# Kernel optimization log

Measured on AMD Instinct MI355X. Metric: run time of the kernel, lower is better.

## Reference

```python
import jax, jax.numpy as jnp
import numpy as np

MIN_, MAX_, KSZ, IGNORE_IDX = 10, 10, 3, -255
B, H, W = 256, 256, 256
LI_MAX_ITERS = 64


def setup_inputs() -> dict:
    key = jax.random.key(0)
    x = jax.random.uniform(key, (B, 1, H, W), dtype=jnp.float32)
    return {"x": x}


def _otsu(hist):
    # hist: [256] counts. Returns Otsu threshold (bin value); fg = img > t.
    bins = jnp.arange(256, dtype=jnp.float32)
    w0 = jnp.cumsum(hist)[:-1]
    w1 = hist.sum() - w0
    s0 = jnp.cumsum(hist * bins)[:-1]
    s_tot = (hist * bins).sum()
    m0 = s0 / jnp.maximum(w0, 1e-12)
    m1 = (s_tot - s0) / jnp.maximum(w1, 1e-12)
    var_b = w0 * w1 * (m0 - m1) ** 2
    return jnp.argmax(var_b).astype(jnp.float32)


def _li(hist, init_t):
    # Histogram-based Li iterative minimum cross-entropy threshold
    # (skimage.filters.threshold_li with initial_guess=init_t).
    bins = jnp.arange(256, dtype=jnp.float32)
    img_min = jnp.min(jnp.where(hist > 0, bins, 255.0))
    vals = bins - img_min  # shift so values >= 0 (as skimage does)
    csum = jnp.cumsum(hist)
    cvsum = jnp.cumsum(hist * vals)
    n_tot, s_tot = csum[-1], cvsum[-1]
    tol = 0.5  # integer image -> half the minimal value spacing

    def body(state):
        t_curr, _, i = state
        # background: img <= t_curr + img_min
        idx = jnp.clip(jnp.floor(t_curr + img_min).astype(jnp.int32), 0, 255)
        n_back, s_back = csum[idx], cvsum[idx]
        n_fore, s_fore = n_tot - n_back, s_tot - s_back
        mean_back = jnp.where(n_back > 0, s_back / jnp.maximum(n_back, 1.0), 0.0)
        mean_fore = s_fore / jnp.maximum(n_fore, 1.0)
        eps = 1e-12
        t_next = (mean_back - mean_fore) / (
            jnp.log(jnp.maximum(mean_back, eps)) - jnp.log(jnp.maximum(mean_fore, eps)))
        t_next = jnp.where(mean_back < eps, mean_fore / 2.0, t_next)
        return (t_next, t_curr, i + 1)

    def cond(state):
        t_curr, t_prev, i = state
        return (jnp.abs(t_curr - t_prev) > tol) & (i < LI_MAX_ITERS)

    t0 = init_t - img_min
    t_fin, _, _ = jax.lax.while_loop(cond, body, (t0, t0 + 10.0, 0))
    return t_fin + img_min


def _sample_mask(key, region, k):
    # Uniform sampling without replacement of up to k pixels from region
    # (bool [H,W]) via random-score top-k (equiv. to torch.multinomial
    # with uniform probs, w/o replacement).
    flat = region.reshape(-1)
    scores = jnp.where(flat, jax.random.uniform(key, (flat.shape[0],)), -1.0)
    top, idx = jax.lax.top_k(scores, k)
    valid = (top >= 0.0).astype(jnp.int32)
    mask = jnp.zeros(flat.shape[0], jnp.int32).at[idx].max(valid)
    return mask.reshape(region.shape)


def _dilate(m):
    # kornia dilation with ones (KSZ,KSZ) kernel on a 0/1 mask == max filter.
    return jax.lax.reduce_window(m, 0, jax.lax.max, (KSZ, KSZ), (1, 1), "SAME")


def _per_image(img_u8, key_fg, key_bg):
    # img_u8: [H,W] int32 in [0,255]
    hist = jnp.zeros(256, jnp.float32).at[img_u8.ravel()].add(1.0)
    otsu = jnp.clip(_otsu(hist), 1.0, 254.0)  # clamp 0->1, 255->254
    li_t = _li(hist, otsu)
    roi = img_u8.astype(jnp.float32) > li_t

    fg = _sample_mask(key_fg, roi, MAX_)
    bg = _sample_mask(key_bg, jnp.logical_not(roi), MIN_)
    if KSZ > 1:
        fg = _dilate(fg)
        bg = _dilate(bg)

    overlap = (fg + bg) == 2
    fg = jnp.where(overlap, 0, fg)
    bg = jnp.where(overlap, 0, bg)

    seeds = jnp.full((H, W), IGNORE_IDX, jnp.int32)
    seeds = jnp.where(bg == 1, 0, seeds)
    seeds = jnp.where(fg == 1, 1, seeds)
    return seeds


def reference(x):
    b = x.shape[0]
    # (cam*255).astype(uint8): truncation, cam in [0,1]
    img = jnp.clip(jnp.floor(x[:, 0] * 255.0), 0, 255).astype(jnp.int32)
    keys = jax.random.split(jax.random.key(1), (b, 2))
    return jax.vmap(_per_image)(img, keys[:, 0], keys[:, 1])
```

## Files before the change

kernel.cpp:

```cpp
#include <hip/hip_runtime.h>
#include <stdint.h>

#define NPIX 65536
#define IGN (-255)
#define CAP 768
#define HPART 16384
#define SCRI4 4608

__device__ __forceinline__ uint32_t rotl32(uint32_t v, uint32_t r){ return (v<<r)|(v>>(32u-r)); }

__device__ __forceinline__ void tf2x32(uint32_t k0, uint32_t k1, uint32_t x0, uint32_t x1,
                                       uint32_t &o0, uint32_t &o1){
  uint32_t k2 = k0 ^ k1 ^ 0x1BD11BDAu;
  x0 += k0; x1 += k1;
#define TFR(r) { x0 += x1; x1 = rotl32(x1,(r)); x1 ^= x0; }
  TFR(13u) TFR(15u) TFR(26u) TFR(6u)   x0 += k1; x1 += k2 + 1u;
  TFR(17u) TFR(29u) TFR(16u) TFR(24u)  x0 += k2; x1 += k0 + 2u;
  TFR(13u) TFR(15u) TFR(26u) TFR(6u)   x0 += k0; x1 += k1 + 3u;
  TFR(17u) TFR(29u) TFR(16u) TFR(24u)  x0 += k1; x1 += k2 + 4u;
  TFR(13u) TFR(15u) TFR(26u) TFR(6u)   x0 += k2; x1 += k0 + 5u;
#undef TFR
  o0 = x0; o1 = x1;
}

__device__ __forceinline__ unsigned long long packCand(uint32_t bits, uint32_t pix){
  float f = __uint_as_float((bits >> 9) | 0x3f800000u) - 1.0f;
  uint32_t u = __float_as_uint(f) ^ 0x80000000u;
  return ((unsigned long long)u << 32) | (unsigned long long)(0xFFFFFFFFu - pix);
}

__device__ __forceinline__ void t10_insert(unsigned long long* l, unsigned long long c){
  if (c > l[9]) {
    l[9] = c;
#pragma unroll
    for (int i = 9; i > 0; --i){
      unsigned long long a = l[i-1], b2 = l[i];
      if (b2 > a){ l[i-1] = b2; l[i] = a; }
    }
  }
}

__global__ __launch_bounds__(256, 8)
void k1_stream(const float* __restrict__ x, int* __restrict__ out){
  const int blk = blockIdx.x;
  const int b = blk >> 3, j8 = blk & 7;
  const int tid = threadIdx.x;
  const float4* x4 = (const float4*)(x + (size_t)b * NPIX);
  int* base = out + (size_t)b * NPIX;
  int4* o4 = (int4*)base;

  __shared__ uint32_t histR[1024];
#pragma unroll
  for (int k = 0; k < 4; ++k) histR[tid + 256*k] = 0u;
  __syncthreads();

  const int4 f4 = make_int4(IGN, IGN, IGN, IGN);
  const uint32_t c4 = (uint32_t)(tid & 3);
#pragma unroll
  for (int jj = 0; jj < 8; ++jj){
    int i4 = j8*2048 + jj*256 + tid;
    float4 v = x4[i4];
    uint32_t u0 = (uint32_t)min(max((int)floorf(v.x*255.0f),0),255);
    uint32_t u1 = (uint32_t)min(max((int)floorf(v.y*255.0f),0),255);
    uint32_t u2 = (uint32_t)min(max((int)floorf(v.z*255.0f),0),255);
    uint32_t u3 = (uint32_t)min(max((int)floorf(v.w*255.0f),0),255);
    base[i4] = (int)(u0 | (u1<<8) | (u2<<16) | (u3<<24));
    if (i4 >= SCRI4) o4[i4] = f4;
    atomicAdd(&histR[(u0<<2)|c4],1u); atomicAdd(&histR[(u1<<2)|c4],1u);
    atomicAdd(&histR[(u2<<2)|c4],1u); atomicAdd(&histR[(u3<<2)|c4],1u);
  }
  __syncthreads();
  uint32_t s = histR[4*tid] + histR[4*tid+1] + histR[4*tid+2] + histR[4*tid+3];
  base[HPART + j8*256 + tid] = (int)s;
}

__global__ __launch_bounds__(1024, 4)
void k2_final(int* __restrict__ out){
  const int b = blockIdx.x;
  const int tid = threadIdx.x;
  int* meta = out + (size_t)b * NPIX;
  int* outb = meta;

  __shared__ float csum[256], cvsum[256];
  __shared__ int s_imin, s_qthr, s_nroi;
  __shared__ unsigned long long s_best;
  __shared__ uint32_t s_kw[4];
  __shared__ unsigned long long buf[2][CAP];
  __shared__ int s_cnt[2], s_fail[2], s_np[2];
  __shared__ unsigned long long s_top[2][64][10];
  __shared__ unsigned long long s_top2[2][8][10];
  __shared__ int s_pr[2][10], s_pc[2][10];

  if (tid == 0){ s_imin = 255; s_best = 0ull; }
  if (tid < 2){
    uint32_t o0, o1;
    tf2x32(0u, 1u, 0u, (uint32_t)(2*b + tid), o0, o1);
    s_kw[2*tid] = o0; s_kw[2*tid+1] = o1;
    s_cnt[tid] = 0;
  }
  __syncthreads();

  int h = 0;
  if (tid < 256){
#pragma unroll
    for (int j = 0; j < 8; ++j) h += meta[HPART + j*256 + tid];
    if (h) atomicMin(&s_imin, tid);
  }
  __syncthreads();
  const float img_min = (float)s_imin;
  if (tid < 256){
    csum[tid]  = (float)h;
    cvsum[tid] = (float)h * ((float)tid - img_min);
  }
  __syncthreads();
  for (int off = 1; off < 256; off <<= 1){
    float a = 0.f, c2 = 0.f;
    if (tid < 256 && tid >= off){ a = csum[tid-off]; c2 = cvsum[tid-off]; }
    __syncthreads();
    if (tid < 256 && tid >= off){ csum[tid] += a; cvsum[tid] += c2; }
    __syncthreads();
  }

  {
    float s_tot_o = cvsum[255] + img_min * csum[255];
    if (tid < 255){
      float w0 = csum[tid];
      float w1 = 65536.0f - w0;
      float cs = cvsum[tid] + img_min * csum[tid];
      float m0 = cs / fmaxf(w0, 1e-12f);
      float m1 = (s_tot_o - cs) / fmaxf(w1, 1e-12f);
      float d = m0 - m1;
      float vb = (w0*w1) * (d*d);
      unsigned long long pk =
        ((unsigned long long)__float_as_uint(vb) << 32) | (unsigned long long)(255 - tid);
      atomicMax(&s_best, pk);
    }
  }
  __syncthreads();

  if (tid == 0){
    int bestIdx = 255 - (int)(s_best & 0xFFFFFFFFull);
    float otsu = fminf(fmaxf((float)bestIdx, 1.0f), 254.0f);
    float n_tot = csum[255], s_tot = cvsum[255];
    float t_curr = otsu - img_min, t_prev = t_curr + 10.0f;
    int it = 0;
    while (fabsf(t_curr - t_prev) > 0.5f && it < 64){
      int idx = min(max((int)floorf(t_curr + img_min), 0), 255);
      float n_back = csum[idx], s_back = cvsum[idx];
      float n_fore = n_tot - n_back, s_fore = s_tot - s_back;
      float mean_back = (n_back > 0.0f) ? (s_back / fmaxf(n_back, 1.0f)) : 0.0f;
      float mean_fore = s_fore / fmaxf(n_fore, 1.0f);
      float t_next = (mean_back - mean_fore) /
                     (logf(fmaxf(mean_back, 1e-12f)) - logf(fmaxf(mean_fore, 1e-12f)));
      if (mean_back < 1e-12f) t_next = mean_fore * 0.5f;
      t_prev = t_curr; t_curr = t_next; ++it;
    }
    float lit = t_curr + img_min;
    int qthr;
    if (!(lit == lit)) qthr = 256;
    else               qthr = (int)floorf(lit) + 1;
    s_qthr = qthr;
    int nlo = (qthr <= 0) ? 0 : (int)csum[min(qthr, 256) - 1];
    s_nroi = NPIX - nlo;
  }
  __syncthreads();

  const int qthr = s_qthr;
  const uint32_t fk0 = s_kw[0], fk1 = s_kw[1], bk0 = s_kw[2], bk1 = s_kw[3];
  const int4* u4 = (const int4*)meta;
  int4 w0 = u4[tid], w1 = u4[tid + 1024], w2 = u4[tid + 2048], w3 = u4[tid + 3072];
#pragma unroll
  for (int k = 0; k < 4; ++k){
    int4 w = (k == 0) ? w0 : (k == 1) ? w1 : (k == 2) ? w2 : w3;
    uint32_t pb = (uint32_t)(16*(tid + 1024*k));
    const uint32_t words[4] = {(uint32_t)w.x,(uint32_t)w.y,(uint32_t)w.z,(uint32_t)w.w};
#pragma unroll
    for (int m = 0; m < 4; ++m){
      uint32_t pk = words[m];
#pragma unroll
      for (int s = 0; s < 4; ++s){
        int q = (int)((pk >> (8*s)) & 255u);
        bool r = (q >= qthr);
        uint32_t pix = pb + (uint32_t)(4*m + s);
        uint32_t o0, o1;
        tf2x32(r ? fk0 : bk0, r ? fk1 : bk1, 0u, pix, o0, o1);
        uint32_t bits = o0 ^ o1;
        if (bits >= 0xFF000000u){
          int r2 = r ? 0 : 1;
          int idx = atomicAdd(&s_cnt[r2], 1);
          if (idx < CAP) buf[r2][idx] = packCand(bits, pix);
        }
      }
    }
  }
  __syncthreads();

  if (tid < 2){
    int rs = tid ? (NPIX - s_nroi) : s_nroi;
    int cc = s_cnt[tid];
    s_fail[tid] = (cc > CAP) || (cc < 10 && cc != rs);
  }
  __syncthreads();

  const int wv = tid >> 6, lane = tid & 63;
  if (wv < 2){
    const int r2 = wv;
    unsigned long long t[10];
#pragma unroll
    for (int i = 0; i < 10; ++i) t[i] = 0ull;
    if (!s_fail[r2]){
      int n = min(s_cnt[r2], CAP);
      for (int i = lane; i < n; i += 64) t10_insert(t, buf[r2][i]);
    } else {
      const uint32_t kk0 = s_kw[2*r2], kk1 = s_kw[2*r2+1];
      for (int k = 0; k < 1024; ++k){
        uint32_t pix = (uint32_t)(lane + 64*k);
        int q = (int)(((uint32_t)meta[pix >> 2] >> (8*(pix & 3u))) & 255u);
        bool r = (q >= qthr);
        if (r == (r2 == 0)){
          uint32_t o0, o1; tf2x32(kk0, kk1, 0u, pix, o0, o1);
          t10_insert(t, packCand(o0 ^ o1, pix));
        }
      }
    }
#pragma unroll
    for (int i = 0; i < 10; ++i) s_top[r2][lane][i] = t[i];
  }
  __syncthreads();
  if (wv < 2 && lane < 8){
    unsigned long long t[10];
#pragma unroll
    for (int i = 0; i < 10; ++i) t[i] = 0ull;
    for (int l2 = 0; l2 < 8; ++l2)
#pragma unroll
      for (int i = 0; i < 10; ++i) t10_insert(t, s_top[wv][lane*8 + l2][i]);
#pragma unroll
    for (int i = 0; i < 10; ++i) s_top2[wv][lane][i] = t[i];
  }
  __syncthreads();
  if (wv < 2 && lane == 0){
    unsigned long long t[10];
#pragma unroll
    for (int i = 0; i < 10; ++i) t[i] = 0ull;
    for (int l2 = 0; l2 < 8; ++l2)
#pragma unroll
      for (int i = 0; i < 10; ++i) t10_insert(t, s_top2[wv][l2][i]);
    int np = 0;
    for (int i = 0; i < 10; ++i){
      if (t[i]){
        uint32_t pix = 0xFFFFFFFFu - (uint32_t)(t[i] & 0xFFFFFFFFull);
        s_pr[wv][np] = (int)(pix >> 8);
        s_pc[wv][np] = (int)(pix & 255u);
        ++np;
      }
    }
    s_np[wv] = np;
  }
  __syncthreads();

  const int4 f4 = make_int4(IGN, IGN, IGN, IGN);
#pragma unroll
  for (int k = 0; k < 5; ++k){
    int idx = tid + 1024*k;
    if (idx < SCRI4) ((int4*)meta)[idx] = f4;
  }
  __syncthreads();

  const int nfg = s_np[0], nbg = s_np[1];
  const int npts = nfg + nbg;
  if (tid < npts*9){
    int k = tid / 9, d = tid - k*9;
    int pr = (k < nfg) ? s_pr[0][k] : s_pr[1][k - nfg];
    int pc = (k < nfg) ? s_pc[0][k] : s_pc[1][k - nfg];
    pr += d/3 - 1; pc += d%3 - 1;
    if (pr >= 0 && pr < 256 && pc >= 0 && pc < 256){
      bool fgd = false, bgd = false;
      for (int i = 0; i < nfg; ++i) fgd |= (abs(pr - s_pr[0][i]) <= 1) && (abs(pc - s_pc[0][i]) <= 1);
      for (int i = 0; i < nbg; ++i) bgd |= (abs(pr - s_pr[1][i]) <= 1) && (abs(pc - s_pc[1][i]) <= 1);
      int val = (fgd && bgd) ? IGN : (fgd ? 1 : 0);
      outb[pr*256 + pc] = val;
    }
  }
}

extern "C" void kernel_launch(void* const* d_in, const int* in_sizes, int n_in,
                              void* d_out, int out_size, void* d_ws, size_t ws_size,
                              hipStream_t stream) {
  const float* x = (const float*)d_in[0];
  int* out = (int*)d_out;
  int B = in_sizes[0] / NPIX;
  k1_stream<<<8*B, 256, 0, stream>>>(x, out);
  k2_final <<<B,  1024, 0, stream>>>(out);
}
```

Baseline: 184.1 us.

## Compute histogram scan, Otsu and Li thresholds in a single wavefront

The histogram merge, prefix scan, Otsu argmax and image-minimum reduction move from a 256-thread block-wide Hillis-Steele scan, with many __syncthreads and shared-memory atomics, into one 64-lane wavefront. Each lane handles four bins, and the work uses wave shuffles for the scan and reductions. This removes about 18 block barriers and the shared atomics from the serial threshold phase that every block waits on. The pixel loop also stops loading all four int4 words up front and keeps the outer loop rolled, which lowers register pressure but may reduce memory-level parallelism.

```diff
diff --git a/kernel.cpp b/kernel.cpp
--- a/kernel.cpp
+++ b/kernel.cpp
@@ -82,8 +82,7 @@
   int* outb = meta;
 
   __shared__ float csum[256], cvsum[256];
-  __shared__ int s_imin, s_qthr, s_nroi;
-  __shared__ unsigned long long s_best;
+  __shared__ int s_qthr, s_nroi;
   __shared__ uint32_t s_kw[4];
   __shared__ unsigned long long buf[2][CAP];
   __shared__ int s_cnt[2], s_fail[2], s_np[2];
@@ -91,97 +90,116 @@
   __shared__ unsigned long long s_top2[2][8][10];
   __shared__ int s_pr[2][10], s_pc[2][10];
 
-  if (tid == 0){ s_imin = 255; s_best = 0ull; }
   if (tid < 2){
     uint32_t o0, o1;
     tf2x32(0u, 1u, 0u, (uint32_t)(2*b + tid), o0, o1);
     s_kw[2*tid] = o0; s_kw[2*tid+1] = o1;
     s_cnt[tid] = 0;
   }
-  __syncthreads();
-
-  int h = 0;
-  if (tid < 256){
-#pragma unroll
-    for (int j = 0; j < 8; ++j) h += meta[HPART + j*256 + tid];
-    if (h) atomicMin(&s_imin, tid);
-  }
-  __syncthreads();
-  const float img_min = (float)s_imin;
-  if (tid < 256){
-    csum[tid]  = (float)h;
-    cvsum[tid] = (float)h * ((float)tid - img_min);
-  }
-  __syncthreads();
-  for (int off = 1; off < 256; off <<= 1){
-    float a = 0.f, c2 = 0.f;
-    if (tid < 256 && tid >= off){ a = csum[tid-off]; c2 = cvsum[tid-off]; }
-    __syncthreads();
-    if (tid < 256 && tid >= off){ csum[tid] += a; cvsum[tid] += c2; }
-    __syncthreads();
-  }
-
-  {
-    float s_tot_o = cvsum[255] + img_min * csum[255];
-    if (tid < 255){
-      float w0 = csum[tid];
-      float w1 = 65536.0f - w0;
-      float cs = cvsum[tid] + img_min * csum[tid];
-      float m0 = cs / fmaxf(w0, 1e-12f);
-      float m1 = (s_tot_o - cs) / fmaxf(w1, 1e-12f);
-      float d = m0 - m1;
-      float vb = (w0*w1) * (d*d);
-      unsigned long long pk =
-        ((unsigned long long)__float_as_uint(vb) << 32) | (unsigned long long)(255 - tid);
-      atomicMax(&s_best, pk);
-    }
-  }
-  __syncthreads();
-
-  if (tid == 0){
-    int bestIdx = 255 - (int)(s_best & 0xFFFFFFFFull);
-    float otsu = fminf(fmaxf((float)bestIdx, 1.0f), 254.0f);
-    float n_tot = csum[255], s_tot = cvsum[255];
-    float t_curr = otsu - img_min, t_prev = t_curr + 10.0f;
-    int it = 0;
-    while (fabsf(t_curr - t_prev) > 0.5f && it < 64){
-      int idx = min(max((int)floorf(t_curr + img_min), 0), 255);
-      float n_back = csum[idx], s_back = cvsum[idx];
-      float n_fore = n_tot - n_back, s_fore = s_tot - s_back;
-      float mean_back = (n_back > 0.0f) ? (s_back / fmaxf(n_back, 1.0f)) : 0.0f;
-      float mean_fore = s_fore / fmaxf(n_fore, 1.0f);
-      float t_next = (mean_back - mean_fore) /
-                     (logf(fmaxf(mean_back, 1e-12f)) - logf(fmaxf(mean_fore, 1e-12f)));
-      if (mean_back < 1e-12f) t_next = mean_fore * 0.5f;
-      t_prev = t_curr; t_curr = t_next; ++it;
-    }
-    float lit = t_curr + img_min;
-    int qthr;
-    if (!(lit == lit)) qthr = 256;
-    else               qthr = (int)floorf(lit) + 1;
-    s_qthr = qthr;
-    int nlo = (qthr <= 0) ? 0 : (int)csum[min(qthr, 256) - 1];
-    s_nroi = NPIX - nlo;
+
+  if (tid < 64){
+    const int lane = tid;
+    int h0 = 0, h1 = 0, h2 = 0, h3 = 0;
+    for (int j = 0; j < 8; ++j){
+      const int4 p = *(const int4*)&meta[HPART + j*256 + 4*lane];
+      h0 += p.x; h1 += p.y; h2 += p.z; h3 += p.w;
+    }
+    int cand = 256;
+    if (h3) cand = 4*lane + 3;
+    if (h2) cand = 4*lane + 2;
+    if (h1) cand = 4*lane + 1;
+    if (h0) cand = 4*lane + 0;
+    for (int off = 32; off; off >>= 1) cand = min(cand, __shfl_xor(cand, off));
+    const float img_min = (float)cand;
+    float c0 = (float)h0, c1 = c0 + h1, c2 = c1 + h2, c3 = c2 + h3;
+    float bv = 4.0f*lane - img_min;
+    float v0 = h0*bv;
+    float v1 = v0 + h1*(bv + 1.0f);
+    float v2 = v1 + h2*(bv + 2.0f);
+    float v3 = v2 + h3*(bv + 3.0f);
+    float cc = c3, vv = v3;
+    for (int off = 1; off < 64; off <<= 1){
+      float a = __shfl_up(cc, off), b2 = __shfl_up(vv, off);
+      if (lane >= off){ cc += a; vv += b2; }
+    }
+    const float cexc = cc - c3, vexc = vv - v3;
+    const float cs0 = cexc+c0, cs1 = cexc+c1, cs2 = cexc+c2, cs3 = cexc+c3;
+    const float vs0 = vexc+v0, vs1 = vexc+v1, vs2 = vexc+v2, vs3 = vexc+v3;
+    csum[4*lane]   = cs0; csum[4*lane+1]  = cs1;
+    csum[4*lane+2] = cs2; csum[4*lane+3]  = cs3;
+    cvsum[4*lane]   = vs0; cvsum[4*lane+1] = vs1;
+    cvsum[4*lane+2] = vs2; cvsum[4*lane+3] = vs3;
+    const float ctot = __shfl(cc, 63), vtot = __shfl(vv, 63);
+    const float s_tot_o = vtot + img_min * ctot;
+    unsigned long long best = 0ull;
+#define OTSU_BIN(CS, VS, J)                                              \
+    { int bin = 4*lane + (J);                                            \
+      if (bin < 255){                                                    \
+        float w0 = (CS);                                                 \
+        float w1 = 65536.0f - w0;                                        \
+        float cs = (VS) + img_min * (CS);                                \
+        float m0 = cs / fmaxf(w0, 1e-12f);                               \
+        float m1 = (s_tot_o - cs) / fmaxf(w1, 1e-12f);                   \
+        float d = m0 - m1;                                               \
+        float vb = (w0*w1) * (d*d);                                      \
+        unsigned long long pk =                                          \
+          ((unsigned long long)__float_as_uint(vb) << 32) |              \
+           (unsigned long long)(255 - bin);                              \
+        if (pk > best) best = pk;                                        \
+      } }
+    OTSU_BIN(cs0, vs0, 0) OTSU_BIN(cs1, vs1, 1)
+    OTSU_BIN(cs2, vs2, 2) OTSU_BIN(cs3, vs3, 3)
+#undef OTSU_BIN
+    for (int off = 32; off; off >>= 1){
+      unsigned int hi = (unsigned int)(best >> 32), lo = (unsigned int)best;
+      unsigned int hio = (unsigned int)__shfl_xor((int)hi, off);
+      unsigned int loo = (unsigned int)__shfl_xor((int)lo, off);
+      unsigned long long ob = ((unsigned long long)hio << 32) | loo;
+      if (ob > best) best = ob;
+    }
+    if (lane == 0){
+      int bestIdx = 255 - (int)(best & 0xFFFFFFFFull);
+      float otsu = fminf(fmaxf((float)bestIdx, 1.0f), 254.0f);
+      float n_tot = ctot, s_tot = vtot;
+      float t_curr = otsu - img_min, t_prev = t_curr + 10.0f;
+      int it = 0;
+      while (fabsf(t_curr - t_prev) > 0.5f && it < 64){
+        int idx = min(max((int)floorf(t_curr + img_min), 0), 255);
+        float n_back = csum[idx], s_back = cvsum[idx];
+        float n_fore = n_tot - n_back, s_fore = s_tot - s_back;
+        float mean_back = (n_back > 0.0f) ? (s_back / fmaxf(n_back, 1.0f)) : 0.0f;
+        float mean_fore = s_fore / fmaxf(n_fore, 1.0f);
+        float t_next = (mean_back - mean_fore) /
+                       (logf(fmaxf(mean_back, 1e-12f)) - logf(fmaxf(mean_fore, 1e-12f)));
+        if (mean_back < 1e-12f) t_next = mean_fore * 0.5f;
+        t_prev = t_curr; t_curr = t_next; ++it;
+      }
+      float lit = t_curr + img_min;
+      int qthr;
+      if (!(lit == lit)) qthr = 256;
+      else               qthr = (int)floorf(lit) + 1;
+      s_qthr = qthr;
+      int nlo = (qthr <= 0) ? 0 : (int)csum[min(qthr, 256) - 1];
+      s_nroi = NPIX - nlo;
+    }
   }
   __syncthreads();
 
   const int qthr = s_qthr;
   const uint32_t fk0 = s_kw[0], fk1 = s_kw[1], bk0 = s_kw[2], bk1 = s_kw[3];
   const int4* u4 = (const int4*)meta;
-  int4 w0 = u4[tid], w1 = u4[tid + 1024], w2 = u4[tid + 2048], w3 = u4[tid + 3072];
-#pragma unroll
   for (int k = 0; k < 4; ++k){
-    int4 w = (k == 0) ? w0 : (k == 1) ? w1 : (k == 2) ? w2 : w3;
-    uint32_t pb = (uint32_t)(16*(tid + 1024*k));
-    const uint32_t words[4] = {(uint32_t)w.x,(uint32_t)w.y,(uint32_t)w.z,(uint32_t)w.w};
+    int4 w = u4[tid + 1024*k];
+    uint32_t pw0 = (uint32_t)(16*(tid + 1024*k));
 #pragma unroll
     for (int m = 0; m < 4; ++m){
-      uint32_t pk = words[m];
+      uint32_t pk = (m==0)?(uint32_t)w.x:(m==1)?(uint32_t)w.y:(m==2)?(uint32_t)w.z:(uint32_t)w.w;
+      uint32_t pb = pw0 + (uint32_t)(4*m);
 #pragma unroll
       for (int s = 0; s < 4; ++s){
         int q = (int)((pk >> (8*s)) & 255u);
         bool r = (q >= qthr);
-        uint32_t pix = pb + (uint32_t)(4*m + s);
+        uint32_t pix = pb + (uint32_t)s;
         uint32_t o0, o1;
         tf2x32(r ? fk0 : bk0, r ? fk1 : bk1, 0u, pix, o0, o1);
         uint32_t bits = o0 ^ o1;
```

New measurement: 177.7 us. 1.04x faster.
